# Optimization experiments

Hardware: AMD Instinct MI355X
Metric: run time of the kernel (lower is better)

Reference implementation:

```python
import jax, jax.numpy as jnp
import numpy as np

B, H, L, D = 2, 16, 2048, 128

def setup_inputs() -> dict:
    key = jax.random.key(0)
    kq, kk, kv = jax.random.split(key, 3)
    Q = jax.random.normal(kq, (B, H, L, D), dtype=jnp.float32)
    K = jax.random.normal(kk, (B, H, L, D), dtype=jnp.float32)
    V = jax.random.normal(kv, (B, H, L, D), dtype=jnp.float32)
    # causal mask: True where attention is allowed
    mask = jnp.broadcast_to(jnp.tril(jnp.ones((L, L), dtype=bool)), (B, H, L, L))
    return {"Q": Q, "K": K, "V": V, "mask": mask}

def reference(Q, K, V, mask):
    d_k = Q.shape[-1]
    scale = 1.0 / jnp.sqrt(jnp.asarray(d_k, dtype=Q.dtype))
    # [B,H,Lq,Lk] score matrix (naive materialization, as in the original)
    scores = jnp.einsum('bhqd,bhkd->bhqk', Q, K) * scale
    scores = jnp.where(mask, scores, -jnp.inf)
    attn = jax.nn.softmax(scores, axis=-1)
    return jnp.einsum('bhqk,bhkd->bhqd', attn, V)
```

## Files before the change

### kernel.cpp

```cpp
#include <hip/hip_runtime.h>
#include <hip/hip_bf16.h>

namespace {

constexpr int Bc = 2, Hc = 16, Lc = 2048, Dc = 128;
constexpr int QBLK = 64, KVBLK = 64;
constexpr int BH  = Bc * Hc;
constexpr int NQT = Lc / QBLK;
constexpr int NKT = Lc / KVBLK;
constexpr float SCALE = 0.08838834764831845f * 1.4426950408889634f;

using f32x4  = __attribute__((ext_vector_type(4))) float;
using short8 = __attribute__((ext_vector_type(8))) short;

union FragU { short8 v; short4 h[2]; };

__device__ inline short f2bf(float f) {
  unsigned u = __builtin_bit_cast(unsigned, f);
  u += 0x7fffu + ((u >> 16) & 1u);
  return (short)(u >> 16);
}

__device__ inline void gload_lds16(const short* g, short* l) {
  __builtin_amdgcn_global_load_lds(
      (const __attribute__((address_space(1))) void*)g,
      (__attribute__((address_space(3))) void*)l, 16, 0, 0);
}

__global__ __launch_bounds__(256) void conv_k(const float* __restrict__ Kg,
                                              short* __restrict__ Kw) {
  int tid = blockIdx.x * 256 + threadIdx.x;
  int x   = tid & 15;
  int row = (tid >> 4) & 63;
  int tb  = tid >> 10;
  int xs  = x ^ (row & 7);
  const float* src = Kg + ((size_t)tb * 64 + row) * 128 + xs * 8;
  float4 a = *(const float4*)src;
  float4 b = *(const float4*)(src + 4);
  short8 v;
  v[0] = f2bf(a.x); v[1] = f2bf(a.y); v[2] = f2bf(a.z); v[3] = f2bf(a.w);
  v[4] = f2bf(b.x); v[5] = f2bf(b.y); v[6] = f2bf(b.z); v[7] = f2bf(b.w);
  *(short8*)(Kw + (size_t)tb * 8192 + row * 128 + x * 8) = v;
}

__global__ __launch_bounds__(256) void conv_v(const float* __restrict__ Vg,
                                              short* __restrict__ Vw) {
  __shared__ short Vs[64 * 130];
  int tb  = blockIdx.x;
  int tid = threadIdx.x;
  const float* vt = Vg + (size_t)tb * 8192;
#pragma unroll
  for (int p = 0; p < 8; ++p) {
    int g  = p * 256 + tid;
    int kv = g >> 5;
    int c4 = g & 31;
    float4 v = *((const float4*)vt + g);
    short* d = &Vs[kv * 130 + c4 * 4];
    d[0] = f2bf(v.x); d[1] = f2bf(v.y); d[2] = f2bf(v.z); d[3] = f2bf(v.w);
  }
  __syncthreads();
#pragma unroll
  for (int p = 0; p < 4; ++p) {
    int g = p * 256 + tid;
    int d = g >> 3;
    int x = g & 7;
    int kv0 = (x ^ (d & 7)) * 8;
    short8 o;
#pragma unroll
    for (int j = 0; j < 8; ++j) o[j] = Vs[(kv0 + j) * 130 + d];
    *(short8*)(Vw + (size_t)tb * 8192 + d * 64 + x * 8) = o;
  }
}

__global__ __launch_bounds__(256, 2) void attn_fwd2(
    const float* __restrict__ Qg, const short* __restrict__ Kw,
    const short* __restrict__ Vw, float* __restrict__ Og) {

  __shared__ __align__(16) short lds[2][2][8192];

  const int tid  = threadIdx.x;
  const int wave = tid >> 6;
  const int lane = tid & 63;
  const int lg   = lane >> 4;
  const int lr   = lane & 15;
  const int sw   = (lr & 7) << 4;

  const int bid = blockIdx.x;
  const int bh  = bid & (BH - 1);
  const int qt  = (NQT - 1) - (bid >> 5);
  const int q0w = qt * QBLK + wave * 16;

  const float* Qp = Qg + (size_t)bh * Lc * Dc;
  float*       Op = Og + (size_t)bh * Lc * Dc;
  const short* Kwp = Kw + (size_t)bh * NKT * 8192;
  const short* Vwp = Vw + (size_t)bh * NKT * 8192;

  short8 qf[4];
  {
    const float* qrow = Qp + (size_t)(q0w + lr) * Dc;
#pragma unroll
    for (int dc = 0; dc < 4; ++dc) {
      float4 a = *(const float4*)(qrow + dc * 32 + lg * 4);
      float4 b = *(const float4*)(qrow + dc * 32 + 16 + lg * 4);
      short8 v;
      v[0] = f2bf(a.x * SCALE); v[1] = f2bf(a.y * SCALE);
      v[2] = f2bf(a.z * SCALE); v[3] = f2bf(a.w * SCALE);
      v[4] = f2bf(b.x * SCALE); v[5] = f2bf(b.y * SCALE);
      v[6] = f2bf(b.z * SCALE); v[7] = f2bf(b.w * SCALE);
      qf[dc] = v;
    }
  }

  const f32x4 zero4 = {0.f, 0.f, 0.f, 0.f};
  float m_run = -1e30f, l_run = 0.0f;
  f32x4 oacc[8];
#pragma unroll
  for (int dt = 0; dt < 8; ++dt) oacc[dt] = zero4;

  const int ntiles = qt + 1;

  auto stage = [&](int t, int b) {
    const short* gk = Kwp + (size_t)t * 8192 + wave * 2048 + lane * 8;
    const short* gv = Vwp + (size_t)t * 8192 + wave * 2048 + lane * 8;
    short* lk = &lds[b][0][wave * 2048];
    short* lv = &lds[b][1][wave * 2048];
#pragma unroll
    for (int i = 0; i < 4; ++i) gload_lds16(gk + i * 512, lk + i * 512);
#pragma unroll
    for (int i = 0; i < 4; ++i) gload_lds16(gv + i * 512, lv + i * 512);
  };

  stage(0, 0);

  for (int t = 0; t < ntiles; ++t) {
    const int cur = t & 1;
    __builtin_amdgcn_s_barrier();
    if (t + 1 < ntiles) {
      stage(t + 1, cur ^ 1);
      asm volatile("s_waitcnt vmcnt(8)" ::: "memory");
    } else {
      asm volatile("s_waitcnt vmcnt(0)" ::: "memory");
    }
    __builtin_amdgcn_s_barrier();
    __builtin_amdgcn_sched_barrier(0);

    const short* Kl = &lds[cur][0][0];
    const short* Vl = &lds[cur][1][0];

    f32x4 st[4];
#pragma unroll
    for (int mt = 0; mt < 4; ++mt) st[mt] = zero4;
    __builtin_amdgcn_s_setprio(1);
#pragma unroll
    for (int dc = 0; dc < 4; ++dc) {
#pragma unroll
      for (int mt = 0; mt < 4; ++mt) {
        int rowb = (mt * 16 + lr) * 256;
        FragU a;
        a.h[0] = *(const short4*)((const char*)Kl + rowb + ((dc * 64      + lg * 8) ^ sw));
        a.h[1] = *(const short4*)((const char*)Kl + rowb + ((dc * 64 + 32 + lg * 8) ^ sw));
        st[mt] = __builtin_amdgcn_mfma_f32_16x16x32_bf16(a.v, qf[dc], st[mt], 0, 0, 0);
      }
    }
    __builtin_amdgcn_s_setprio(0);

    if (t == ntiles - 1) {
      const int qg = q0w + lr;
      const int kv0 = t * KVBLK;
#pragma unroll
      for (int mt = 0; mt < 4; ++mt)
#pragma unroll
        for (int r = 0; r < 4; ++r)
          if (kv0 + mt * 16 + lg * 4 + r > qg) st[mt][r] = -1e30f;
    }

    float mx = st[0][0];
#pragma unroll
    for (int mt = 0; mt < 4; ++mt)
#pragma unroll
      for (int r = 0; r < 4; ++r) mx = fmaxf(mx, st[mt][r]);
    mx = fmaxf(mx, __shfl_xor(mx, 16));
    mx = fmaxf(mx, __shfl_xor(mx, 32));

    if (!__all(mx - m_run <= 8.0f)) {
      float mnew = fmaxf(m_run, mx);
      float corr = exp2f(m_run - mnew);
      m_run = mnew;
      l_run *= corr;
#pragma unroll
      for (int r = 0; r < 4; ++r) {
        float c = __shfl(corr, (lane & 48) + lg * 4 + r);
#pragma unroll
        for (int dt = 0; dt < 8; ++dt) oacc[dt][r] *= c;
      }
    }

    float pr[4][4];
    float rs = 0.0f;
#pragma unroll
    for (int mt = 0; mt < 4; ++mt)
#pragma unroll
      for (int r = 0; r < 4; ++r) {
        float e = exp2f(st[mt][r] - m_run);
        pr[mt][r] = e;
        rs += e;
      }
    rs += __shfl_xor(rs, 16);
    rs += __shfl_xor(rs, 32);
    l_run += rs;

    short8 pf[2];
#pragma unroll
    for (int c = 0; c < 2; ++c) {
      short8 v;
      v[0] = f2bf(pr[2 * c][0]);     v[1] = f2bf(pr[2 * c][1]);
      v[2] = f2bf(pr[2 * c][2]);     v[3] = f2bf(pr[2 * c][3]);
      v[4] = f2bf(pr[2 * c + 1][0]); v[5] = f2bf(pr[2 * c + 1][1]);
      v[6] = f2bf(pr[2 * c + 1][2]); v[7] = f2bf(pr[2 * c + 1][3]);
      pf[c] = v;
    }

    __builtin_amdgcn_s_setprio(1);
#pragma unroll
    for (int dt = 0; dt < 8; ++dt) {
      int rowb = (dt * 16 + lr) * 128;
#pragma unroll
      for (int c = 0; c < 2; ++c) {
        FragU b;
        b.h[0] = *(const short4*)((const char*)Vl + rowb + ((c * 64      + lg * 8) ^ sw));
        b.h[1] = *(const short4*)((const char*)Vl + rowb + ((c * 64 + 32 + lg * 8) ^ sw));
        oacc[dt] = __builtin_amdgcn_mfma_f32_16x16x32_bf16(pf[c], b.v, oacc[dt], 0, 0, 0);
      }
    }
    __builtin_amdgcn_s_setprio(0);
  }

#pragma unroll
  for (int r = 0; r < 4; ++r) {
    float li = __shfl(l_run, (lane & 48) + lg * 4 + r);
    float inv = 1.0f / li;
    float* orow = Op + (size_t)(q0w + lg * 4 + r) * Dc;
#pragma unroll
    for (int dt = 0; dt < 8; ++dt)
      orow[dt * 16 + lr] = oacc[dt][r] * inv;
  }
}

__device__ inline unsigned packbf(float a, float b) {
  return (unsigned)(unsigned short)f2bf(a) | ((unsigned)(unsigned short)f2bf(b) << 16);
}

__global__ __launch_bounds__(256, 2) void attn_fb(
    const float* __restrict__ Qg, const float* __restrict__ Kg,
    const float* __restrict__ Vg, float* __restrict__ Og) {
  __shared__ __align__(16) short Klds[KVBLK * Dc];
  __shared__ __align__(16) short Vt[Dc * 68];
  const int tid = threadIdx.x, wave = tid >> 6, lane = tid & 63;
  const int lg = lane >> 4, lr = lane & 15;
  const int bid = blockIdx.x;
  const int bh = bid & (BH - 1);
  const int qt = (NQT - 1) - (bid >> 5);
  const int q0w = qt * QBLK + wave * 16;
  const float* Qp = Qg + (size_t)bh * Lc * Dc;
  const float* Kp = Kg + (size_t)bh * Lc * Dc;
  const float* Vp = Vg + (size_t)bh * Lc * Dc;
  float* Op = Og + (size_t)bh * Lc * Dc;
  short8 qf[4];
  {
    const float* qrow = Qp + (size_t)(q0w + lr) * Dc;
#pragma unroll
    for (int dc = 0; dc < 4; ++dc) {
      float4 a = *(const float4*)(qrow + dc * 32 + lg * 4);
      float4 b = *(const float4*)(qrow + dc * 32 + 16 + lg * 4);
      short8 v;
      v[0]=f2bf(a.x*SCALE); v[1]=f2bf(a.y*SCALE); v[2]=f2bf(a.z*SCALE); v[3]=f2bf(a.w*SCALE);
      v[4]=f2bf(b.x*SCALE); v[5]=f2bf(b.y*SCALE); v[6]=f2bf(b.z*SCALE); v[7]=f2bf(b.w*SCALE);
      qf[dc] = v;
    }
  }
  const f32x4 zero4 = {0.f,0.f,0.f,0.f};
  float m_run = -1e30f, l_run = 0.0f;
  f32x4 oacc[8];
#pragma unroll
  for (int dt = 0; dt < 8; ++dt) oacc[dt] = zero4;
  const int ntiles = qt + 1, c4 = tid & 31, rK = tid >> 5;
  for (int t = 0; t < ntiles; ++t) {
    const int kv0 = t * KVBLK;
    __syncthreads();
#pragma unroll
    for (int p = 0; p < 8; ++p) {
      int row = rK + p * 8;
      float4 k4 = *(const float4*)(Kp + (size_t)(kv0 + row) * Dc + c4 * 4);
      short4 pk; pk.x=f2bf(k4.x); pk.y=f2bf(k4.y); pk.z=f2bf(k4.z); pk.w=f2bf(k4.w);
      *(short4*)((char*)Klds + row * 256 + ((c4 * 8) ^ ((row & 7) << 4))) = pk;
    }
#pragma unroll
    for (int p = 0; p < 4; ++p) {
      int r0 = rK * 2 + p * 16;
      float4 v0 = *(const float4*)(Vp + (size_t)(kv0 + r0) * Dc + c4 * 4);
      float4 v1 = *(const float4*)(Vp + (size_t)(kv0 + r0 + 1) * Dc + c4 * 4);
      char* vb = (char*)Vt + r0 * 2;
      *(unsigned*)(vb + (c4*4+0)*136) = packbf(v0.x, v1.x);
      *(unsigned*)(vb + (c4*4+1)*136) = packbf(v0.y, v1.y);
      *(unsigned*)(vb + (c4*4+2)*136) = packbf(v0.z, v1.z);
      *(unsigned*)(vb + (c4*4+3)*136) = packbf(v0.w, v1.w);
    }
    __syncthreads();
    f32x4 st[4];
#pragma unroll
    for (int mt = 0; mt < 4; ++mt) st[mt] = zero4;
#pragma unroll
    for (int dc = 0; dc < 4; ++dc)
#pragma unroll
      for (int mt = 0; mt < 4; ++mt) {
        int row = mt * 16 + lr, sw2 = (row & 7) << 4;
        FragU a;
        a.h[0] = *(short4*)((char*)Klds + row*256 + ((dc*64      + lg*8) ^ sw2));
        a.h[1] = *(short4*)((char*)Klds + row*256 + ((dc*64 + 32 + lg*8) ^ sw2));
        st[mt] = __builtin_amdgcn_mfma_f32_16x16x32_bf16(a.v, qf[dc], st[mt], 0, 0, 0);
      }
    if (t == ntiles - 1) {
      const int qg = q0w + lr;
#pragma unroll
      for (int mt = 0; mt < 4; ++mt)
#pragma unroll
        for (int r = 0; r < 4; ++r)
          if (kv0 + mt * 16 + lg * 4 + r > qg) st[mt][r] = -1e30f;
    }
    float mx = st[0][0];
#pragma unroll
    for (int mt = 0; mt < 4; ++mt)
#pragma unroll
      for (int r = 0; r < 4; ++r) mx = fmaxf(mx, st[mt][r]);
    mx = fmaxf(mx, __shfl_xor(mx, 16));
    mx = fmaxf(mx, __shfl_xor(mx, 32));
    float mnew = fmaxf(m_run, mx);
    float corr = exp2f(m_run - mnew);
    m_run = mnew;
    float pr[4][4]; float rs = 0.0f;
#pragma unroll
    for (int mt = 0; mt < 4; ++mt)
#pragma unroll
      for (int r = 0; r < 4; ++r) { float e = exp2f(st[mt][r] - mnew); pr[mt][r] = e; rs += e; }
    rs += __shfl_xor(rs, 16);
    rs += __shfl_xor(rs, 32);
    l_run = l_run * corr + rs;
#pragma unroll
    for (int r = 0; r < 4; ++r) {
      float c = __shfl(corr, (lane & 48) + lg * 4 + r);
#pragma unroll
      for (int dt = 0; dt < 8; ++dt) oacc[dt][r] *= c;
    }
    short8 pf[2];
#pragma unroll
    for (int c = 0; c < 2; ++c) {
      short8 v;
      v[0]=f2bf(pr[2*c][0]); v[1]=f2bf(pr[2*c][1]); v[2]=f2bf(pr[2*c][2]); v[3]=f2bf(pr[2*c][3]);
      v[4]=f2bf(pr[2*c+1][0]); v[5]=f2bf(pr[2*c+1][1]); v[6]=f2bf(pr[2*c+1][2]); v[7]=f2bf(pr[2*c+1][3]);
      pf[c] = v;
    }
#pragma unroll
    for (int dt = 0; dt < 8; ++dt) {
      int rowb = (dt * 16 + lr) * 136;
#pragma unroll
      for (int c = 0; c < 2; ++c) {
        FragU b;
        b.h[0] = *(short4*)((char*)Vt + rowb + c*64      + lg*8);
        b.h[1] = *(short4*)((char*)Vt + rowb + c*64 + 32 + lg*8);
        oacc[dt] = __builtin_amdgcn_mfma_f32_16x16x32_bf16(pf[c], b.v, oacc[dt], 0, 0, 0);
      }
    }
  }
#pragma unroll
  for (int r = 0; r < 4; ++r) {
    float li = __shfl(l_run, (lane & 48) + lg * 4 + r);
    float inv = 1.0f / li;
    float* orow = Op + (size_t)(q0w + lg * 4 + r) * Dc;
#pragma unroll
    for (int dt = 0; dt < 8; ++dt) orow[dt * 16 + lr] = oacc[dt][r] * inv;
  }
}

}

extern "C" void kernel_launch(void* const* d_in, const int* in_sizes, int n_in,
                              void* d_out, int out_size, void* d_ws, size_t ws_size,
                              hipStream_t stream) {
  const float* Q = (const float*)d_in[0];
  const float* K = (const float*)d_in[1];
  const float* V = (const float*)d_in[2];
  float* O = (float*)d_out;
  const size_t elems = (size_t)BH * Lc * Dc;
  const size_t need  = 2 * elems * sizeof(short);
  if (ws_size >= need) {
    short* Kw = (short*)d_ws;
    short* Vw = Kw + elems;
    conv_k<<<dim3(4096), dim3(256), 0, stream>>>(K, Kw);
    conv_v<<<dim3(1024), dim3(256), 0, stream>>>(V, Vw);
    attn_fwd2<<<dim3(BH * NQT), dim3(256), 0, stream>>>(Q, Kw, Vw, O);
  } else {
    attn_fb<<<dim3(BH * NQT), dim3(256), 0, stream>>>(Q, K, V, O);
  }
}
```

Baseline: 105.5 us.

## Double query tile to 128 rows with 8 waves sharing each staged KV tile

The attention kernel now processes 128-query tiles with 512 threads (8 waves), so each K/V tile staged in LDS is reused by twice as many query rows, halving global K/V traffic per query. The block-to-tile mapping interleaves heavy and light causal tiles, and waves whose rows lie entirely before a KV tile skip its compute but still join the barriers. The exp/bf16 packing is also fused into a single loop. In exchange there are fewer blocks (512), a larger causal imbalance inside a block, and the launch bound asks for 4 blocks of 512 threads per CU, which increases register pressure.

```diff
diff --git a/kernel.cpp b/kernel.cpp
--- a/kernel.cpp
+++ b/kernel.cpp
@@ -4,10 +4,11 @@
 namespace {
 
 constexpr int Bc = 2, Hc = 16, Lc = 2048, Dc = 128;
-constexpr int QBLK = 64, KVBLK = 64;
+constexpr int KVBLK = 64;
 constexpr int BH  = Bc * Hc;
-constexpr int NQT = Lc / QBLK;
 constexpr int NKT = Lc / KVBLK;
+constexpr int QB3 = 128;
+constexpr int NQT3 = Lc / QB3;
 constexpr float SCALE = 0.08838834764831845f * 1.4426950408889634f;
 
 using f32x4  = __attribute__((ext_vector_type(4))) float;
@@ -72,7 +73,7 @@
   }
 }
 
-__global__ __launch_bounds__(256, 2) void attn_fwd2(
+__global__ __launch_bounds__(512, 4) void attn_fwd3(
     const float* __restrict__ Qg, const short* __restrict__ Kw,
     const short* __restrict__ Vw, float* __restrict__ Og) {
 
@@ -87,8 +88,9 @@
 
   const int bid = blockIdx.x;
   const int bh  = bid & (BH - 1);
-  const int qt  = (NQT - 1) - (bid >> 5);
-  const int q0w = qt * QBLK + wave * 16;
+  const int r5  = bid >> 5;
+  const int qt  = (bid < 256) ? (NQT3 - 1 - r5) : (r5 - 8);
+  const int q0w = qt * QB3 + wave * 16;
 
   const float* Qp = Qg + (size_t)bh * Lc * Dc;
   float*       Op = Og + (size_t)bh * Lc * Dc;
@@ -117,17 +119,15 @@
 #pragma unroll
   for (int dt = 0; dt < 8; ++dt) oacc[dt] = zero4;
 
-  const int ntiles = qt + 1;
+  const int ntiles = 2 * (qt + 1);
 
   auto stage = [&](int t, int b) {
-    const short* gk = Kwp + (size_t)t * 8192 + wave * 2048 + lane * 8;
-    const short* gv = Vwp + (size_t)t * 8192 + wave * 2048 + lane * 8;
-    short* lk = &lds[b][0][wave * 2048];
-    short* lv = &lds[b][1][wave * 2048];
-#pragma unroll
-    for (int i = 0; i < 4; ++i) gload_lds16(gk + i * 512, lk + i * 512);
-#pragma unroll
-    for (int i = 0; i < 4; ++i) gload_lds16(gv + i * 512, lv + i * 512);
+    const short* gk = Kwp + (size_t)t * 8192 + tid * 8;
+    const short* gv = Vwp + (size_t)t * 8192 + tid * 8;
+    short* lk = &lds[b][0][tid * 8];
+    short* lv = &lds[b][1][tid * 8];
+    gload_lds16(gk, lk);            gload_lds16(gk + 4096, lk + 4096);
+    gload_lds16(gv, lv);            gload_lds16(gv + 4096, lv + 4096);
   };
 
   stage(0, 0);
@@ -137,12 +137,15 @@
     __builtin_amdgcn_s_barrier();
     if (t + 1 < ntiles) {
       stage(t + 1, cur ^ 1);
-      asm volatile("s_waitcnt vmcnt(8)" ::: "memory");
+      asm volatile("s_waitcnt vmcnt(4)" ::: "memory");
     } else {
       asm volatile("s_waitcnt vmcnt(0)" ::: "memory");
     }
     __builtin_amdgcn_s_barrier();
     __builtin_amdgcn_sched_barrier(0);
+
+    const int kv0 = t * KVBLK;
+    if (q0w + 15 < kv0) continue;
 
     const short* Kl = &lds[cur][0][0];
     const short* Vl = &lds[cur][1][0];
@@ -164,9 +167,8 @@
     }
     __builtin_amdgcn_s_setprio(0);
 
-    if (t == ntiles - 1) {
+    if (t >= 2 * qt) {
       const int qg = q0w + lr;
-      const int kv0 = t * KVBLK;
 #pragma unroll
       for (int mt = 0; mt < 4; ++mt)
 #pragma unroll
@@ -195,30 +197,24 @@
       }
     }
 
-    float pr[4][4];
     float rs = 0.0f;
-#pragma unroll
-    for (int mt = 0; mt < 4; ++mt)
-#pragma unroll
-      for (int r = 0; r < 4; ++r) {
-        float e = exp2f(st[mt][r] - m_run);
-        pr[mt][r] = e;
-        rs += e;
-      }
+    short8 pf[2];
+#pragma unroll
+    for (int c = 0; c < 2; ++c) {
+      short8 v;
+#pragma unroll
+      for (int j = 0; j < 4; ++j) {
+        float e = exp2f(st[2 * c][j] - m_run);     rs += e; v[j]     = f2bf(e);
+      }
+#pragma unroll
+      for (int j = 0; j < 4; ++j) {
+        float e = exp2f(st[2 * c + 1][j] - m_run); rs += e; v[4 + j] = f2bf(e);
+      }
+      pf[c] = v;
+    }
     rs += __shfl_xor(rs, 16);
     rs += __shfl_xor(rs, 32);
     l_run += rs;
-
-    short8 pf[2];
-#pragma unroll
-    for (int c = 0; c < 2; ++c) {
-      short8 v;
-      v[0] = f2bf(pr[2 * c][0]);     v[1] = f2bf(pr[2 * c][1]);
-      v[2] = f2bf(pr[2 * c][2]);     v[3] = f2bf(pr[2 * c][3]);
-      v[4] = f2bf(pr[2 * c + 1][0]); v[5] = f2bf(pr[2 * c + 1][1]);
-      v[6] = f2bf(pr[2 * c + 1][2]); v[7] = f2bf(pr[2 * c + 1][3]);
-      pf[c] = v;
-    }
 
     __builtin_amdgcn_s_setprio(1);
 #pragma unroll
@@ -259,8 +255,8 @@
   const int lg = lane >> 4, lr = lane & 15;
   const int bid = blockIdx.x;
   const int bh = bid & (BH - 1);
-  const int qt = (NQT - 1) - (bid >> 5);
-  const int q0w = qt * QBLK + wave * 16;
+  const int qt = 31 - (bid >> 5);
+  const int q0w = qt * 64 + wave * 16;
   const float* Qp = Qg + (size_t)bh * Lc * Dc;
   const float* Kp = Kg + (size_t)bh * Lc * Dc;
   const float* Vp = Vg + (size_t)bh * Lc * Dc;
@@ -397,8 +393,8 @@
     short* Vw = Kw + elems;
     conv_k<<<dim3(4096), dim3(256), 0, stream>>>(K, Kw);
     conv_v<<<dim3(1024), dim3(256), 0, stream>>>(V, Vw);
-    attn_fwd2<<<dim3(BH * NQT), dim3(256), 0, stream>>>(Q, Kw, Vw, O);
+    attn_fwd3<<<dim3(BH * NQT3), dim3(512), 0, stream>>>(Q, Kw, Vw, O);
   } else {
-    attn_fb<<<dim3(BH * NQT), dim3(256), 0, stream>>>(Q, K, V, O);
-  }
-}
+    attn_fb<<<dim3(BH * NKT), dim3(256), 0, stream>>>(Q, K, V, O);
+  }
+}
```

Result: slower. 115.2 us (+9.2%).
